# Kernel tuning notes

Measured on AMD Instinct MI355X. Metric: run time of the kernel, lower is better.

Reference implementation:

```python
import jax, jax.numpy as jnp
import numpy as np

EMBED_DIM = 1024
NUM_HEADS = 16
HEAD_DIM = EMBED_DIM // NUM_HEADS
B, QL, CL = 2, 2048, 2048


def setup_inputs() -> dict:
    key = jax.random.key(0)
    ks = jax.random.split(key, 10)
    s = 1.0 / np.sqrt(EMBED_DIM)  # torch Linear default init scale (approx)
    inp = {
        "query": jax.random.normal(ks[0], (B, QL, EMBED_DIM), jnp.float32),
        "context": jax.random.normal(ks[1], (B, CL, EMBED_DIM), jnp.float32),
        "Wq": jax.random.normal(ks[2], (EMBED_DIM, EMBED_DIM), jnp.float32) * s,
        "bq": jnp.zeros((EMBED_DIM,), jnp.float32),
        "Wk": jax.random.normal(ks[3], (EMBED_DIM, EMBED_DIM), jnp.float32) * s,
        "bk": jnp.zeros((EMBED_DIM,), jnp.float32),
        "Wv": jax.random.normal(ks[4], (EMBED_DIM, EMBED_DIM), jnp.float32) * s,
        "bv": jnp.zeros((EMBED_DIM,), jnp.float32),
        "Wo": jax.random.normal(ks[5], (EMBED_DIM, EMBED_DIM), jnp.float32) * s,
        "bo": jnp.zeros((EMBED_DIM,), jnp.float32),
    }
    return inp


def reference(query, context, Wq, bq, Wk, bk, Wv, bv, Wo, bo):
    b, ql, _ = query.shape
    cl = context.shape[1]
    # projections (torch Linear: x @ W.T + b; here W stored as (in, out) so x @ W + b)
    Q = (query @ Wq + bq).reshape(b, ql, NUM_HEADS, HEAD_DIM).transpose(0, 2, 1, 3)
    K = (context @ Wk + bk).reshape(b, cl, NUM_HEADS, HEAD_DIM).transpose(0, 2, 1, 3)
    V = (context @ Wv + bv).reshape(b, cl, NUM_HEADS, HEAD_DIM).transpose(0, 2, 1, 3)
    # scores [b, h, ql, cl]
    scores = jnp.einsum("bhqd,bhkd->bhqk", Q, K) / np.sqrt(HEAD_DIM).astype(np.float32)
    probs = jax.nn.softmax(scores, axis=-1)
    # dropout=0.0 (eval): identity
    attended = jnp.einsum("bhqk,bhkd->bhqd", probs, V)
    attended = attended.transpose(0, 2, 1, 3).reshape(b, ql, EMBED_DIM)
    return attended @ Wo + bo
```

## Files before the change

kernel.cpp:

```cpp
#include <hip/hip_runtime.h>
#include <hip/hip_bf16.h>
#include <stdint.h>

#define EMBED 1024
#define NH 16
#define HD 64
#define BATCH 2
#define QLEN 2048
#define CLEN 2048

typedef short short8 __attribute__((ext_vector_type(8)));
typedef float f32x4 __attribute__((ext_vector_type(4)));
typedef float f32x16 __attribute__((ext_vector_type(16)));
typedef uint32_t u32x4 __attribute__((ext_vector_type(4)));

__device__ __forceinline__ void async_load16(const void* g, void* l) {
    __builtin_amdgcn_global_load_lds((const __attribute__((address_space(1))) void*)g,
                                     (__attribute__((address_space(3))) void*)l, 16, 0, 0);
}

__device__ __forceinline__ uint32_t pack2(float a, float b) {
    float2 f{a, b};
    __hip_bfloat162 t = __float22bfloat162_rn(f);
    uint32_t u;
    __builtin_memcpy(&u, &t, 4);
    return u;
}

__global__ void prep(const float* __restrict__ query, const float* __restrict__ context,
                     __hip_bfloat16* __restrict__ qbf, __hip_bfloat16* __restrict__ cbf,
                     const float* __restrict__ W0, const float* __restrict__ W1,
                     const float* __restrict__ W2, const float* __restrict__ W3,
                     __hip_bfloat16* __restrict__ T0, __hip_bfloat16* __restrict__ T1,
                     __hip_bfloat16* __restrict__ T2, __hip_bfloat16* __restrict__ T3) {
    const int y = blockIdx.y;
    const int tid = threadIdx.x;
    if (y < 2) {
        const float* src = y ? context : query;
        __hip_bfloat16* dst = y ? cbf : qbf;
#pragma unroll
        for (int k = 0; k < 4; k++) {
            const int i = (blockIdx.x * 1024 + k * 256 + tid) * 4;
            float4 v = *(const float4*)(src + i);
            __hip_bfloat16 h[4];
            h[0] = __float2bfloat16(v.x);
            h[1] = __float2bfloat16(v.y);
            h[2] = __float2bfloat16(v.z);
            h[3] = __float2bfloat16(v.w);
            *(ushort4*)(dst + i) = *(const ushort4*)h;
        }
    } else {
        const int z = y - 2;
        const float* W = z == 0 ? W0 : z == 1 ? W1 : z == 2 ? W2 : W3;
        __hip_bfloat16* Wt = z == 0 ? T0 : z == 1 ? T1 : z == 2 ? T2 : T3;
        __shared__ float t[32][33];
        const int tx = tid & 31, ty = tid >> 5;
        const int n0 = (blockIdx.x & 31) * 32, k0 = (blockIdx.x >> 5) * 32;
#pragma unroll
        for (int r = 0; r < 4; r++)
            t[ty * 4 + r][tx] = W[(size_t)(k0 + ty * 4 + r) * EMBED + n0 + tx];
        __syncthreads();
#pragma unroll
        for (int r = 0; r < 4; r++)
            Wt[(size_t)(n0 + ty * 4 + r) * EMBED + k0 + tx] = __float2bfloat16(t[tx][ty * 4 + r]);
    }
}

__device__ __forceinline__ void gemm128_acc(
    const __hip_bfloat16* __restrict__ A, const __hip_bfloat16* __restrict__ Bt,
    int m0, int n0, __hip_bfloat16* As, __hip_bfloat16* Bs, f32x4 acc[4][4]) {
    const int K = EMBED;
    const int tid = threadIdx.x;
    const int wave = __builtin_amdgcn_readfirstlane(tid >> 6);
    const int lane = tid & 63, l15 = lane & 15, quad = lane >> 4;
    const int wm = (wave >> 1) * 64, wn = (wave & 1) * 64;
    const int srow = tid >> 2, sseg = (tid & 3) * 8;
    for (int k0 = 0; k0 < K; k0 += 32) {
        __syncthreads();
#pragma unroll
        for (int s = 0; s < 2; s++) {
            async_load16(A + (size_t)(m0 + s * 64 + srow) * K + k0 + sseg,
                         As + (size_t)(s * 256 + wave * 64) * 8);
            async_load16(Bt + (size_t)(n0 + s * 64 + srow) * K + k0 + sseg,
                         Bs + (size_t)(s * 256 + wave * 64) * 8);
        }
        __syncthreads();
        short8 af[4], bf[4];
#pragma unroll
        for (int t = 0; t < 4; t++) {
            af[t] = *(const short8*)(As + (wm + t * 16 + l15) * 32 + quad * 8);
            bf[t] = *(const short8*)(Bs + (wn + t * 16 + l15) * 32 + quad * 8);
        }
#pragma unroll
        for (int mt = 0; mt < 4; mt++)
#pragma unroll
            for (int nt = 0; nt < 4; nt++)
                acc[mt][nt] = __builtin_amdgcn_mfma_f32_16x16x32_bf16(af[mt], bf[nt], acc[mt][nt], 0, 0, 0);
    }
}

__global__ __launch_bounds__(256, 3) void proj128(
    const __hip_bfloat16* __restrict__ qbf, const __hip_bfloat16* __restrict__ cbf,
    const __hip_bfloat16* __restrict__ Wqt, const __hip_bfloat16* __restrict__ Wkvt,
    const float* __restrict__ bq, const float* __restrict__ bk, const float* __restrict__ bv,
    __hip_bfloat16* __restrict__ Qp, __hip_bfloat16* __restrict__ Kp, __hip_bfloat16* __restrict__ Vtr) {
    __shared__ __hip_bfloat16 As[128 * 32];
    __shared__ __hip_bfloat16 Bs[128 * 32];
    const int blk = blockIdx.x;
    const __hip_bfloat16 *A, *Bt;
    int m0, n0;
    if (blk < 256) {
        A = qbf; Bt = Wqt; m0 = (blk >> 3) * 128; n0 = (blk & 7) * 128;
    } else {
        const int f = blk - 256;
        A = cbf; Bt = Wkvt; m0 = (f >> 4) * 128; n0 = (f & 15) * 128;
    }
    f32x4 acc[4][4] = {};
    gemm128_acc(A, Bt, m0, n0, As, Bs, acc);

    const int tid = threadIdx.x;
    const int wave = __builtin_amdgcn_readfirstlane(tid >> 6);
    const int lane = tid & 63, l15 = lane & 15, quad = lane >> 4;
    const int wm = (wave >> 1) * 64, wn = (wave & 1) * 64;

    if (blk >= 256 && n0 >= 1024) {
        const int cb = n0 - 1024;
        const int b2 = m0 >> 11;
        const int tokbase = (m0 & 2047) + wm;
#pragma unroll
        for (int mt = 0; mt < 4; mt++) {
#pragma unroll
            for (int nt = 0; nt < 4; nt++) {
                const int col = cb + wn + nt * 16 + l15;
                const float bvv = bv[col];
                const int tok = tokbase + mt * 16 + quad * 4;
                __hip_bfloat16 vb[4];
#pragma unroll
                for (int r = 0; r < 4; r++) vb[r] = __float2bfloat16(acc[mt][nt][r] + bvv);
                *(ushort4*)(Vtr + (size_t)(b2 * 1024 + col) * CLEN + tok) = *(const ushort4*)vb;
            }
        }
    } else {
        const float* bias = (blk < 256) ? bq : bk;
        __hip_bfloat16* C = (blk < 256) ? Qp : Kp;
#pragma unroll
        for (int mt = 0; mt < 4; mt++) {
#pragma unroll
            for (int nt = 0; nt < 4; nt++) {
                const int c = n0 + wn + nt * 16 + l15;
                const float bvv = bias[c];
                const int r0 = m0 + wm + mt * 16 + quad * 4;
#pragma unroll
                for (int r = 0; r < 4; r++)
                    C[(size_t)(r0 + r) * 1024 + c] = __float2bfloat16(acc[mt][nt][r] + bvv);
            }
        }
    }
}

__global__ __launch_bounds__(256, 4) void oproj(
    const __hip_bfloat16* __restrict__ A, const __hip_bfloat16* __restrict__ Bt,
    const float* __restrict__ bias, float* __restrict__ C) {
    __shared__ __hip_bfloat16 As[64 * 32];
    __shared__ __hip_bfloat16 Bs[128 * 32];
    const int K = EMBED, N = EMBED;
    const int m0 = blockIdx.y * 64, n0 = blockIdx.x * 128;
    const int tid = threadIdx.x;
    const int wave = __builtin_amdgcn_readfirstlane(tid >> 6);
    const int lane = tid & 63, l15 = lane & 15, quad = lane >> 4;
    const int wm = (wave & 1) * 32, wn = (wave >> 1) * 64;
    const int srow = tid >> 2, sseg = (tid & 3) * 8;
    f32x4 acc[2][4] = {};
    for (int k0 = 0; k0 < K; k0 += 32) {
        __syncthreads();
        async_load16(A + (size_t)(m0 + srow) * K + k0 + sseg, As + (size_t)(wave * 64) * 8);
#pragma unroll
        for (int s = 0; s < 2; s++)
            async_load16(Bt + (size_t)(n0 + s * 64 + srow) * K + k0 + sseg,
                         Bs + (size_t)(s * 256 + wave * 64) * 8);
        __syncthreads();
        short8 af[2], bf[4];
#pragma unroll
        for (int t = 0; t < 2; t++)
            af[t] = *(const short8*)(As + (wm + t * 16 + l15) * 32 + quad * 8);
#pragma unroll
        for (int t = 0; t < 4; t++)
            bf[t] = *(const short8*)(Bs + (wn + t * 16 + l15) * 32 + quad * 8);
#pragma unroll
        for (int mt = 0; mt < 2; mt++)
#pragma unroll
            for (int nt = 0; nt < 4; nt++)
                acc[mt][nt] = __builtin_amdgcn_mfma_f32_16x16x32_bf16(af[mt], bf[nt], acc[mt][nt], 0, 0, 0);
    }
#pragma unroll
    for (int mt = 0; mt < 2; mt++) {
#pragma unroll
        for (int nt = 0; nt < 4; nt++) {
            const int c = n0 + wn + nt * 16 + l15;
            const float bvv = bias[c];
            const int r0 = m0 + wm + mt * 16 + quad * 4;
#pragma unroll
            for (int r = 0; r < 4; r++)
                C[(size_t)(r0 + r) * N + c] = acc[mt][nt][r] + bvv;
        }
    }
}

__global__ __launch_bounds__(256, 4) void flash_attn(
    const __hip_bfloat16* __restrict__ Q, const __hip_bfloat16* __restrict__ K,
    const __hip_bfloat16* __restrict__ Vt, __hip_bfloat16* __restrict__ O) {
    __shared__ __hip_bfloat16 Ks[2][64 * 64];
    __shared__ __hip_bfloat16 Vs[2][64 * 64];
    const int tid = threadIdx.x;
    const int wave = __builtin_amdgcn_readfirstlane(tid >> 6);
    const int wq = wave & 1, wc = wave >> 1;
    const int lane = tid & 63, l31 = lane & 31, hbit = lane >> 5;
    const int b = blockIdx.y >> 4, h = blockIdx.y & 15;
    const int q0 = blockIdx.x * 64;
    const size_t kbase = (size_t)b * CLEN * EMBED + (size_t)h * HD;
    const size_t vtbase = (size_t)((b * NH + h) * HD) * CLEN;
    const int srow8 = lane >> 3;
    const int sg = (lane & 7) ^ srow8;
    __hip_bfloat16* stK = Ks[wc];
    __hip_bfloat16* stV = Vs[wc];

    const __hip_bfloat16* qptr =
        Q + (size_t)(b * QLEN + q0 + wq * 32 + l31) * EMBED + h * HD + hbit * 8;
    short8 qf[4];
#pragma unroll
    for (int t = 0; t < 4; t++) qf[t] = *(const short8*)(qptr + t * 16);

    f32x16 o[2] = {};
    float lsum = 0.f;
    const float CEXP = 0.125f * 1.44269504f;
    const int cbase = wc * (CLEN / 2);

    for (int t = 0; t < 16; ++t) {
        const int c0 = cbase + t * 64;
        __syncthreads();
        if (wq == 0) {
#pragma unroll
            for (int i = 0; i < 8; i++)
                async_load16(K + kbase + (size_t)(c0 + i * 8 + srow8) * EMBED + sg * 8,
                             stK + i * 512);
        } else {
#pragma unroll
            for (int i = 0; i < 8; i++)
                async_load16(Vt + vtbase + (size_t)(i * 8 + srow8) * CLEN + c0 + sg * 8,
                             stV + i * 512);
        }
        __syncthreads();

#pragma unroll
        for (int mc = 0; mc < 2; mc++) {
            const int row = mc * 32 + l31;
            const __hip_bfloat16* kr = stK + row * 64;
            f32x16 s = {};
#pragma unroll
            for (int kc = 0; kc < 4; kc++) {
                short8 kf = *(const short8*)(kr + ((2 * kc + hbit) ^ (row & 7)) * 8);
                s = __builtin_amdgcn_mfma_f32_32x32x16_bf16(kf, qf[kc], s, 0, 0, 0);
            }
            uint32_t dw[8];
#pragma unroll
            for (int i = 0; i < 8; i++) {
                const float p0 = __builtin_amdgcn_exp2f(s[2 * i] * CEXP);
                const float p1 = __builtin_amdgcn_exp2f(s[2 * i + 1] * CEXP);
                lsum += p0 + p1;
                dw[i] = pack2(p0, p1);
            }
#pragma unroll
            for (int tp = 0; tp < 2; tp++) {
                const uint32_t a0 = hbit ? dw[4 * tp + 2] : dw[4 * tp + 0];
                const uint32_t a1 = hbit ? dw[4 * tp + 3] : dw[4 * tp + 1];
                const uint32_t b0 = hbit ? dw[4 * tp + 0] : dw[4 * tp + 2];
                const uint32_t b1 = hbit ? dw[4 * tp + 1] : dw[4 * tp + 3];
                const uint32_t x0 = (uint32_t)__shfl_xor((int)b0, 32);
                const uint32_t x1 = (uint32_t)__shfl_xor((int)b1, 32);
                u32x4 fb;
                fb[0] = hbit ? x0 : a0;
                fb[1] = hbit ? x1 : a1;
                fb[2] = hbit ? a0 : x0;
                fb[3] = hbit ? a1 : x1;
                const short8 pfr = __builtin_bit_cast(short8, fb);
                const int kc2 = mc * 2 + tp;
#pragma unroll
                for (int dm = 0; dm < 2; dm++) {
                    const int vrow = dm * 32 + l31;
                    short8 vf = *(const short8*)(stV + vrow * 64 + ((2 * kc2 + hbit) ^ (vrow & 7)) * 8);
                    o[dm] = __builtin_amdgcn_mfma_f32_32x32x16_bf16(vf, pfr, o[dm], 0, 0, 0);
                }
            }
        }
    }

    __syncthreads();
    float4* scr4 = (float4*)&Ks[0][0];
    float* scrl = (float*)&Vs[0][0];
    if (wc == 1) {
#pragma unroll
        for (int i = 0; i < 8; i++) {
            float4 c4;
            c4.x = o[i >> 2][(i & 3) * 4 + 0];
            c4.y = o[i >> 2][(i & 3) * 4 + 1];
            c4.z = o[i >> 2][(i & 3) * 4 + 2];
            c4.w = o[i >> 2][(i & 3) * 4 + 3];
            scr4[i * 128 + wq * 64 + lane] = c4;
        }
        scrl[wq * 64 + lane] = lsum;
    }
    __syncthreads();
    if (wc == 0) {
        lsum += scrl[wq * 64 + lane];
#pragma unroll
        for (int i = 0; i < 8; i++) {
            float4 p = scr4[i * 128 + wq * 64 + lane];
            o[i >> 2][(i & 3) * 4 + 0] += p.x;
            o[i >> 2][(i & 3) * 4 + 1] += p.y;
            o[i >> 2][(i & 3) * 4 + 2] += p.z;
            o[i >> 2][(i & 3) * 4 + 3] += p.w;
        }
        lsum += __shfl_xor(lsum, 32);
        const float inv = 1.0f / lsum;
        const int q = q0 + wq * 32 + l31;
        __hip_bfloat16* orow = O + (size_t)(b * QLEN + q) * EMBED + h * HD;
#pragma unroll
        for (int dm = 0; dm < 2; dm++) {
#pragma unroll
            for (int g = 0; g < 4; g++) {
                __hip_bfloat16 ob[4];
#pragma unroll
                for (int r = 0; r < 4; r++) ob[r] = __float2bfloat16(o[dm][g * 4 + r] * inv);
                *(ushort4*)(orow + dm * 32 + hbit * 4 + g * 8) = *(const ushort4*)ob;
            }
        }
    }
}

extern "C" void kernel_launch(void* const* d_in, const int* in_sizes, int n_in,
                              void* d_out, int out_size, void* d_ws, size_t ws_size,
                              hipStream_t stream) {
    const float* query = (const float*)d_in[0];
    const float* context = (const float*)d_in[1];
    const float* Wq = (const float*)d_in[2];
    const float* bq = (const float*)d_in[3];
    const float* Wk = (const float*)d_in[4];
    const float* bk = (const float*)d_in[5];
    const float* Wv = (const float*)d_in[6];
    const float* bv = (const float*)d_in[7];
    const float* Wo = (const float*)d_in[8];
    const float* bo = (const float*)d_in[9];
    float* out = (float*)d_out;

    const int NTOK = BATCH * QLEN;
    const int NACT = NTOK * EMBED;
    const int NW = EMBED * EMBED;

    __hip_bfloat16* qbf = (__hip_bfloat16*)d_ws;
    __hip_bfloat16* cbf = qbf + NACT;
    __hip_bfloat16* Wqt = cbf + NACT;
    __hip_bfloat16* Wkt = Wqt + NW;
    __hip_bfloat16* Wvt = Wkt + NW;
    __hip_bfloat16* Wot = Wvt + NW;
    __hip_bfloat16* Qp = Wot + NW;
    __hip_bfloat16* Kp = Qp + NACT;
    __hip_bfloat16* Vtr = Kp + NACT;
    __hip_bfloat16* att = Vtr + NACT;

    prep<<<dim3(1024, 6), 256, 0, stream>>>(query, context, qbf, cbf,
                                            Wq, Wk, Wv, Wo, Wqt, Wkt, Wvt, Wot);

    proj128<<<768, 256, 0, stream>>>(qbf, cbf, Wqt, Wkt, bq, bk, bv, Qp, Kp, Vtr);

    flash_attn<<<dim3(QLEN / 64, BATCH * NH), 256, 0, stream>>>(Qp, Kp, Vtr, att);

    oproj<<<dim3(EMBED / 128, NTOK / 64), 256, 0, stream>>>(att, Wot, bo, out);
}
```

Before: 212.3 us.

## Swizzle block order for XCD locality, prescale Q, use permlane32 swap

Remaps linear block indices in the projection, attention and output kernels so consecutive blocks dispatched to the same XCD work on neighbouring tiles, improving L2 reuse. Folds the softmax scale and log2(e) into the Q projection output so the attention inner loop skips a multiply before exp2. Replaces the cross-half shuffle plus selects used to build the P fragment with the permlane32_swap builtin when available. Prescaling Q before bf16 rounding slightly changes numerics.

Result: faster. 205.6 us (-3.2%).

```diff
diff --git a/kernel.cpp b/kernel.cpp
--- a/kernel.cpp
+++ b/kernel.cpp
@@ -13,6 +13,8 @@
 typedef float f32x4 __attribute__((ext_vector_type(4)));
 typedef float f32x16 __attribute__((ext_vector_type(16)));
 typedef uint32_t u32x4 __attribute__((ext_vector_type(4)));
+
+#define QSCALE 0.18033688f
 
 __device__ __forceinline__ void async_load16(const void* g, void* l) {
     __builtin_amdgcn_global_load_lds((const __attribute__((address_space(1))) void*)g,
@@ -106,7 +108,8 @@
     __hip_bfloat16* __restrict__ Qp, __hip_bfloat16* __restrict__ Kp, __hip_bfloat16* __restrict__ Vtr) {
     __shared__ __hip_bfloat16 As[128 * 32];
     __shared__ __hip_bfloat16 Bs[128 * 32];
-    const int blk = blockIdx.x;
+    const int j = blockIdx.x;
+    const int blk = (j & 7) * 96 + (j >> 3);
     const __hip_bfloat16 *A, *Bt;
     int m0, n0;
     if (blk < 256) {
@@ -141,8 +144,10 @@
             }
         }
     } else {
-        const float* bias = (blk < 256) ? bq : bk;
-        __hip_bfloat16* C = (blk < 256) ? Qp : Kp;
+        const bool isQ = (blk < 256);
+        const float* bias = isQ ? bq : bk;
+        __hip_bfloat16* C = isQ ? Qp : Kp;
+        const float sc = isQ ? QSCALE : 1.0f;
 #pragma unroll
         for (int mt = 0; mt < 4; mt++) {
 #pragma unroll
@@ -152,7 +157,7 @@
                 const int r0 = m0 + wm + mt * 16 + quad * 4;
 #pragma unroll
                 for (int r = 0; r < 4; r++)
-                    C[(size_t)(r0 + r) * 1024 + c] = __float2bfloat16(acc[mt][nt][r] + bvv);
+                    C[(size_t)(r0 + r) * 1024 + c] = __float2bfloat16((acc[mt][nt][r] + bvv) * sc);
             }
         }
     }
@@ -164,7 +169,9 @@
     __shared__ __hip_bfloat16 As[64 * 32];
     __shared__ __hip_bfloat16 Bs[128 * 32];
     const int K = EMBED, N = EMBED;
-    const int m0 = blockIdx.y * 64, n0 = blockIdx.x * 128;
+    const int j = blockIdx.x;
+    const int L = (j & 7) * 64 + (j >> 3);
+    const int m0 = (L >> 3) * 64, n0 = (L & 7) * 128;
     const int tid = threadIdx.x;
     const int wave = __builtin_amdgcn_readfirstlane(tid >> 6);
     const int lane = tid & 63, l15 = lane & 15, quad = lane >> 4;
@@ -215,8 +222,11 @@
     const int wave = __builtin_amdgcn_readfirstlane(tid >> 6);
     const int wq = wave & 1, wc = wave >> 1;
     const int lane = tid & 63, l31 = lane & 31, hbit = lane >> 5;
-    const int b = blockIdx.y >> 4, h = blockIdx.y & 15;
-    const int q0 = blockIdx.x * 64;
+    const int j = blockIdx.x;
+    const int L = (j & 7) * 128 + (j >> 3);
+    const int hy = L >> 5;
+    const int b = hy >> 4, h = hy & 15;
+    const int q0 = (L & 31) * 64;
     const size_t kbase = (size_t)b * CLEN * EMBED + (size_t)h * HD;
     const size_t vtbase = (size_t)((b * NH + h) * HD) * CLEN;
     const int srow8 = lane >> 3;
@@ -232,7 +242,6 @@
 
     f32x16 o[2] = {};
     float lsum = 0.f;
-    const float CEXP = 0.125f * 1.44269504f;
     const int cbase = wc * (CLEN / 2);
 
     for (int t = 0; t < 16; ++t) {
@@ -264,24 +273,37 @@
             uint32_t dw[8];
 #pragma unroll
             for (int i = 0; i < 8; i++) {
-                const float p0 = __builtin_amdgcn_exp2f(s[2 * i] * CEXP);
-                const float p1 = __builtin_amdgcn_exp2f(s[2 * i + 1] * CEXP);
+                const float p0 = __builtin_amdgcn_exp2f(s[2 * i]);
+                const float p1 = __builtin_amdgcn_exp2f(s[2 * i + 1]);
                 lsum += p0 + p1;
                 dw[i] = pack2(p0, p1);
             }
 #pragma unroll
             for (int tp = 0; tp < 2; tp++) {
-                const uint32_t a0 = hbit ? dw[4 * tp + 2] : dw[4 * tp + 0];
-                const uint32_t a1 = hbit ? dw[4 * tp + 3] : dw[4 * tp + 1];
-                const uint32_t b0 = hbit ? dw[4 * tp + 0] : dw[4 * tp + 2];
-                const uint32_t b1 = hbit ? dw[4 * tp + 1] : dw[4 * tp + 3];
-                const uint32_t x0 = (uint32_t)__shfl_xor((int)b0, 32);
-                const uint32_t x1 = (uint32_t)__shfl_xor((int)b1, 32);
                 u32x4 fb;
-                fb[0] = hbit ? x0 : a0;
-                fb[1] = hbit ? x1 : a1;
-                fb[2] = hbit ? a0 : x0;
-                fb[3] = hbit ? a1 : x1;
+#if __has_builtin(__builtin_amdgcn_permlane32_swap)
+                {
+                    auto s02 = __builtin_amdgcn_permlane32_swap(dw[4 * tp + 0], dw[4 * tp + 2], false, false);
+                    auto s13 = __builtin_amdgcn_permlane32_swap(dw[4 * tp + 1], dw[4 * tp + 3], false, false);
+                    fb[0] = s02[0];
+                    fb[1] = s13[0];
+                    fb[2] = s02[1];
+                    fb[3] = s13[1];
+                }
+#else
+                {
+                    const uint32_t a0 = hbit ? dw[4 * tp + 2] : dw[4 * tp + 0];
+                    const uint32_t a1 = hbit ? dw[4 * tp + 3] : dw[4 * tp + 1];
+                    const uint32_t b0 = hbit ? dw[4 * tp + 0] : dw[4 * tp + 2];
+                    const uint32_t b1 = hbit ? dw[4 * tp + 1] : dw[4 * tp + 3];
+                    const uint32_t x0 = (uint32_t)__shfl_xor((int)b0, 32);
+                    const uint32_t x1 = (uint32_t)__shfl_xor((int)b1, 32);
+                    fb[0] = hbit ? x0 : a0;
+                    fb[1] = hbit ? x1 : a1;
+                    fb[2] = hbit ? a0 : x0;
+                    fb[3] = hbit ? a1 : x1;
+                }
+#endif
                 const short8 pfr = __builtin_bit_cast(short8, fb);
                 const int kc2 = mc * 2 + tp;
 #pragma unroll
@@ -372,7 +394,7 @@
 
     proj128<<<768, 256, 0, stream>>>(qbf, cbf, Wqt, Wkt, bq, bk, bv, Qp, Kp, Vtr);
 
-    flash_attn<<<dim3(QLEN / 64, BATCH * NH), 256, 0, stream>>>(Qp, Kp, Vtr, att);
-
-    oproj<<<dim3(EMBED / 128, NTOK / 64), 256, 0, stream>>>(att, Wot, bo, out);
-}
+    flash_attn<<<1024, 256, 0, stream>>>(Qp, Kp, Vtr, att);
+
+    oproj<<<512, 256, 0, stream>>>(att, Wot, bo, out);
+}
```
